# Performance work log

Measured on AMD Instinct MI355X. Metric: run time of the kernel, lower is better.

The kernel has to match this reference:

```python
import jax, jax.numpy as jnp
import numpy as np

N = 10000
E = 160000
IN_DIM = 128
HID = 128
HEADS = 8
INT_DIM = 512
OUT_DIM = 3
NEG_SLOPE = 0.2


def gat_conv(x, src, dst, W, a_src, a_dst, b, heads, ch):
    # x: [N, F_in]; W: [F_in, heads*ch]; a_src/a_dst: [heads, ch]; b: [heads*ch]
    n = x.shape[0]
    h = (x @ W).reshape(n, heads, ch)                      # [N,H,C]
    alpha_src = jnp.einsum('nhc,hc->nh', h, a_src)         # [N,H]
    alpha_dst = jnp.einsum('nhc,hc->nh', h, a_dst)         # [N,H]
    e = jax.nn.leaky_relu(alpha_src[src] + alpha_dst[dst], NEG_SLOPE)  # [E,H]
    # segment softmax over incoming edges of each dst node
    emax = jax.ops.segment_max(e, dst, num_segments=n)     # [N,H]
    ee = jnp.exp(e - emax[dst])
    denom = jax.ops.segment_sum(ee, dst, num_segments=n)   # [N,H]
    alpha = ee / (denom[dst] + 1e-16)                      # [E,H]
    msg = h[src] * alpha[:, :, None]                       # [E,H,C]
    out = jax.ops.segment_sum(msg, dst, num_segments=n)    # [N,H,C]
    return out.reshape(n, heads * ch) + b


def setup_inputs() -> dict:
    key = jax.random.key(0)
    ks = jax.random.split(key, 20)

    def glorot(k, shape):
        fan = shape[0] + shape[-1]
        s = jnp.sqrt(6.0 / fan)
        return jax.random.uniform(k, shape, jnp.float32, -s, s)

    x = jax.random.normal(ks[0], (N, IN_DIM), jnp.float32)
    edge_index = jax.random.randint(ks[1], (2, E), 0, N, jnp.int32)
    return {
        'x': x,
        'edge_index': edge_index,
        'W1': glorot(ks[2], (IN_DIM, HEADS * HID)),
        'a_src1': glorot(ks[3], (HEADS, HID)),
        'a_dst1': glorot(ks[4], (HEADS, HID)),
        'b1': jnp.zeros((HEADS * HID,), jnp.float32),
        'W2': glorot(ks[5], (HEADS * HID, HEADS * HID)),
        'a_src2': glorot(ks[6], (HEADS, HID)),
        'a_dst2': glorot(ks[7], (HEADS, HID)),
        'b2': jnp.zeros((HEADS * HID,), jnp.float32),
        'W3': glorot(ks[8], (HEADS * HID, INT_DIM)),
        'a_src3': glorot(ks[9], (1, INT_DIM)),
        'a_dst3': glorot(ks[10], (1, INT_DIM)),
        'b3': jnp.zeros((INT_DIM,), jnp.float32),
        'Wl': glorot(ks[11], (INT_DIM, INT_DIM)),
        'bl': jnp.zeros((INT_DIM,), jnp.float32),
        'Wc': glorot(ks[12], (INT_DIM, OUT_DIM)),
        'bc': jnp.zeros((OUT_DIM,), jnp.float32),
    }


def reference(x, edge_index, W1, a_src1, a_dst1, b1, W2, a_src2, a_dst2, b2,
              W3, a_src3, a_dst3, b3, Wl, bl, Wc, bc):
    src, dst = edge_index[0], edge_index[1]
    # eval mode: dropout_edge and Dropout are identity
    h = gat_conv(x, src, dst, W1, a_src1, a_dst1, b1, HEADS, HID)
    h = jax.nn.relu(h)
    h = gat_conv(h, src, dst, W2, a_src2, a_dst2, b2, HEADS, HID)
    h = jax.nn.relu(h)
    h = gat_conv(h, src, dst, W3, a_src3, a_dst3, b3, 1, INT_DIM)
    h = jax.nn.relu(h)
    h = jax.nn.relu(h @ Wl + bl)
    return h @ Wc + bc
```

## Files before the change

### kernel.cpp

```cpp
#include <hip/hip_runtime.h>
#include <hip/hip_bf16.h>

#define NN 10000
#define EE 160000
#define IN_DIM 128
#define HID 128
#define HEADS 8
#define F1 (HEADS*HID)
#define INT_DIM 512
#define OUT_DIM 3
#define MPAD 10112

typedef __attribute__((ext_vector_type(4))) float f32x4;
typedef __attribute__((ext_vector_type(8))) _Float16 half8;
typedef __attribute__((ext_vector_type(4))) _Float16 half4;
typedef __attribute__((ext_vector_type(2))) _Float16 half2v;

#define WAVE_SYNC() do { asm volatile("s_waitcnt lgkmcnt(0)" ::: "memory"); \
                         __builtin_amdgcn_sched_barrier(0); } while(0)

__global__ __launch_bounds__(256) void count_kernel(const int* __restrict__ dst, int E, int* __restrict__ cnt){
    int e = blockIdx.x*256 + threadIdx.x;
    if(e < E) atomicAdd(&cnt[dst[e]], 1);
}

__global__ __launch_bounds__(256) void scan_kernel(const int* __restrict__ cnt, int* __restrict__ rowp,
                                                   int* __restrict__ cursor, int n){
    __shared__ int sh[256];
    __shared__ int stotal;
    int t = threadIdx.x;
    if(t==0) stotal = 0;
    __syncthreads();
    for(int base=0; base<n; base+=256){
        int i = base + t;
        int v = (i<n) ? cnt[i] : 0;
        sh[t] = v;
        __syncthreads();
        #pragma unroll
        for(int off=1; off<256; off<<=1){
            int add = (t>=off) ? sh[t-off] : 0;
            __syncthreads();
            sh[t] += add;
            __syncthreads();
        }
        int excl = sh[t] - v;
        if(i<n){ rowp[i] = stotal + excl; cursor[i] = stotal + excl; }
        int chunk_total = sh[255];
        __syncthreads();
        if(t==0) stotal += chunk_total;
        __syncthreads();
    }
    if(t==0) rowp[n] = stotal;
}

__global__ __launch_bounds__(256) void fill_kernel(const int* __restrict__ src, const int* __restrict__ dst,
                                                   int E, int* __restrict__ cursor, int* __restrict__ colsrc){
    int e = blockIdx.x*256 + threadIdx.x;
    if(e < E){
        int d = dst[e];
        int pos = atomicAdd(&cursor[d], 1);
        colsrc[pos] = src[e];
    }
}

__global__ __launch_bounds__(256) void splitT16_kernel(const float* __restrict__ B, _Float16* __restrict__ T,
                                                       int K, int N){
    __shared__ float tile[32][33];
    const int tx = threadIdx.x & 31, ty = threadIdx.x >> 5;
    const int n0 = blockIdx.x * 32, k0 = blockIdx.y * 32;
    #pragma unroll
    for(int i = 0; i < 32; i += 8)
        tile[ty + i][tx] = B[(size_t)(k0 + ty + i) * N + n0 + tx];
    __syncthreads();
    #pragma unroll
    for(int i = 0; i < 32; i += 8){
        int n = ty + i;
        T[(size_t)(n0 + n) * K + k0 + tx] = (_Float16)tile[tx][n];
    }
}

__global__ __launch_bounds__(256) void x16_kernel(const float* __restrict__ x, _Float16* __restrict__ x16, int n4){
    int i = blockIdx.x*256 + threadIdx.x;
    if(i >= n4) return;
    float4 v = ((const float4*)x)[i];
    half4 o = { (_Float16)v.x, (_Float16)v.y, (_Float16)v.z, (_Float16)v.w };
    ((half4*)x16)[i] = o;
}

__global__ __launch_bounds__(256) void aw1_kernel(const float* __restrict__ W1,
                                                  const float* __restrict__ a_src,
                                                  const float* __restrict__ a_dst,
                                                  float* __restrict__ aw){
    int idx = blockIdx.x*256 + threadIdx.x;
    if(idx >= 16*IN_DIM) return;
    int j = idx >> 7, k = idx & 127;
    int hj = j & 7;
    const float* av = (j < 8 ? a_src : a_dst) + hj*HID;
    const float* wr = W1 + (size_t)k*F1 + hj*HID;
    float s = 0.f;
    #pragma unroll 4
    for(int c = 0; c < HID; c++) s += av[c] * wr[c];
    aw[idx] = s;
}

__global__ __launch_bounds__(256) void alpha1_kernel(const float* __restrict__ x,
                                                     const float* __restrict__ aw,
                                                     float* __restrict__ asrc, float* __restrict__ adst){
    __shared__ float xs[16][128];
    __shared__ float aws[16][128];
    int t = threadIdx.x;
    int nb = blockIdx.x * 16;
    for(int i = t; i < 16*128; i += 256){
        xs[i >> 7][i & 127] = x[(size_t)nb*128 + i];
        aws[i >> 7][i & 127] = aw[i];
    }
    __syncthreads();
    int nl = t >> 4, j = t & 15;
    float s = 0.f;
    #pragma unroll 4
    for(int c = 0; c < 128; c++) s += xs[nl][c] * aws[j][c];
    int node = nb + nl;
    if(j < 8) asrc[node*8 + j] = s;
    else      adst[node*8 + (j-8)] = s;
}

__global__ __launch_bounds__(256) void agg1_kernel(const _Float16* __restrict__ x16,
                                                   const float* __restrict__ asrc,
                                                   const float* __restrict__ adst,
                                                   const int* __restrict__ rowp,
                                                   const int* __restrict__ colsrc,
                                                   _Float16* __restrict__ oa){
    const int w = threadIdx.x >> 6, l = threadIdx.x & 63;
    const int node = blockIdx.x*4 + w;
    __shared__ float sh_ee[4][64][8];
    int beg = rowp[node], end = rowp[node+1];
    float rd = adst[node*8 + (l & 7)];
    float acc0[8], acc1[8];
    #pragma unroll
    for(int h=0;h<8;h++){ acc0[h]=0.f; acc1[h]=0.f; }
    float dpart = 0.f;
    for(int base=beg; base<end; base+=64){
        int clen = min(64, end-base);
        WAVE_SYNC();
        int sreg = (l < clen) ? colsrc[base + l] : 0;
        for(int it=l; it<clen*8; it+=64){
            int j = it >> 3;
            int s = colsrc[base + j];
            float e = asrc[s*8 + (l & 7)] + rd;
            e = (e > 0.f) ? e : 0.2f*e;
            float ee = expf(e);
            sh_ee[w][j][l & 7] = ee;
            dpart += ee;
        }
        WAVE_SYNC();
        #pragma unroll 2
        for(int j=0;j<clen;j++){
            int s = __shfl(sreg, j);
            half2v xv = ((const half2v*)(x16 + (size_t)s*128))[l];
            float x0 = (float)xv[0], x1 = (float)xv[1];
            #pragma unroll
            for(int h=0;h<8;h++){
                float wt = sh_ee[w][j][h];
                acc0[h] += wt * x0;
                acc1[h] += wt * x1;
            }
        }
    }
    dpart += __shfl_xor(dpart, 8);
    dpart += __shfl_xor(dpart, 16);
    dpart += __shfl_xor(dpart, 32);
    #pragma unroll
    for(int h=0;h<8;h++){
        float dn = __shfl(dpart, h) + 1e-16f;
        half2v o = { (_Float16)(acc0[h]/dn), (_Float16)(acc1[h]/dn) };
        *(half2v*)(oa + (size_t)node*F1 + h*128 + 2*l) = o;
    }
}

__global__ __launch_bounds__(256) void agg2_kernel(const _Float16* __restrict__ hbuf,
                                                   const float* __restrict__ asrc,
                                                   const float* __restrict__ adst,
                                                   const int* __restrict__ rowp,
                                                   const int* __restrict__ colsrc,
                                                   const float* __restrict__ bias,
                                                   _Float16* __restrict__ oa){
    const int w = threadIdx.x >> 6, l = threadIdx.x & 63;
    const int h = blockIdx.x & 7;
    const int node = (blockIdx.x >> 3)*4 + w;
    const int g = l >> 4, i = l & 15;
    int beg = rowp[node], end = rowp[node+1];
    float rd = adst[node*8 + h];
    float acc[8];
    #pragma unroll
    for(int k=0;k<8;k++) acc[k]=0.f;
    float dpart = 0.f;
    const _Float16* hb = hbuf + h*128 + 8*i;
    for(int base=beg; base<end; base+=64){
        int clen = min(64, end-base);
        int sreg = 0; float eereg = 0.f;
        if(l < clen){
            sreg = colsrc[base + l];
            float e = asrc[sreg*8 + h] + rd;
            e = (e > 0.f) ? e : 0.2f*e;
            eereg = expf(e);
            dpart += eereg;
        }
        int cpad = (clen + 3) & ~3;
        int s0 = __shfl(sreg, g);
        float w0 = __shfl(eereg, g);
        half8 v0 = *(const half8*)(hb + (size_t)s0*F1);
        #pragma unroll 1
        for(int j0=0; j0<cpad; j0+=4){
            half8 nv; float nw = 0.f;
            const bool more = (j0+4 < cpad);
            if(more){
                int ns = __shfl(sreg, j0+4+g);
                nw = __shfl(eereg, j0+4+g);
                nv = *(const half8*)(hb + (size_t)ns*F1);
            }
            #pragma unroll
            for(int k=0;k<8;k++) acc[k] += w0 * (float)v0[k];
            if(more){ v0 = nv; w0 = nw; }
        }
    }
    #pragma unroll
    for(int k=0;k<8;k++){
        acc[k] += __shfl_xor(acc[k], 16);
        acc[k] += __shfl_xor(acc[k], 32);
    }
    #pragma unroll
    for(int off=1; off<64; off<<=1) dpart += __shfl_xor(dpart, off);
    float dn = dpart + 1e-16f;
    if(g == 0){
        const int f = h*128 + 8*i;
        float4 b0 = *(const float4*)(bias + f);
        float4 b1 = *(const float4*)(bias + f + 4);
        float bb[8] = {b0.x,b0.y,b0.z,b0.w, b1.x,b1.y,b1.z,b1.w};
        half8 o;
        #pragma unroll
        for(int k=0;k<8;k++)
            o[k] = (_Float16)fmaxf(acc[k]/dn + bb[k], 0.f);
        *(half8*)(oa + (size_t)node*F1 + f) = o;
    }
}

__global__ __launch_bounds__(256) void agg3_kernel(const _Float16* __restrict__ hbuf,
                                                   const float* __restrict__ asrc,
                                                   const float* __restrict__ adst,
                                                   const int* __restrict__ rowp,
                                                   const int* __restrict__ colsrc,
                                                   const float* __restrict__ bias,
                                                   _Float16* __restrict__ oa){
    const int w = threadIdx.x >> 6, l = threadIdx.x & 63;
    const int i7 = blockIdx.x & 7;
    const int chunk = i7 & 3, sub = i7 >> 2;
    const int node = ((blockIdx.x >> 3)*2 + sub)*4 + w;
    const int g = l >> 4, i = l & 15;
    int beg = rowp[node], end = rowp[node+1];
    float rd = adst[node];
    float acc[8];
    #pragma unroll
    for(int k=0;k<8;k++) acc[k]=0.f;
    float dpart = 0.f;
    const _Float16* hb = hbuf + chunk*128 + 8*i;
    for(int base=beg; base<end; base+=64){
        int clen = min(64, end-base);
        int sreg = 0; float eereg = 0.f;
        if(l < clen){
            sreg = colsrc[base + l];
            float e = asrc[sreg] + rd;
            e = (e > 0.f) ? e : 0.2f*e;
            eereg = expf(e);
            dpart += eereg;
        }
        int cpad = (clen + 3) & ~3;
        int s0 = __shfl(sreg, g);
        float w0 = __shfl(eereg, g);
        half8 v0 = *(const half8*)(hb + (size_t)s0*INT_DIM);
        #pragma unroll 1
        for(int j0=0; j0<cpad; j0+=4){
            half8 nv; float nw = 0.f;
            const bool more = (j0+4 < cpad);
            if(more){
                int ns = __shfl(sreg, j0+4+g);
                nw = __shfl(eereg, j0+4+g);
                nv = *(const half8*)(hb + (size_t)ns*INT_DIM);
            }
            #pragma unroll
            for(int k=0;k<8;k++) acc[k] += w0 * (float)v0[k];
            if(more){ v0 = nv; w0 = nw; }
        }
    }
    #pragma unroll
    for(int k=0;k<8;k++){
        acc[k] += __shfl_xor(acc[k], 16);
        acc[k] += __shfl_xor(acc[k], 32);
    }
    #pragma unroll
    for(int off=1; off<64; off<<=1) dpart += __shfl_xor(dpart, off);
    float dn = dpart + 1e-16f;
    if(g == 0){
        const int f = chunk*128 + 8*i;
        float4 b0 = *(const float4*)(bias + f);
        float4 b1 = *(const float4*)(bias + f + 4);
        float bb[8] = {b0.x,b0.y,b0.z,b0.w, b1.x,b1.y,b1.z,b1.w};
        half8 o;
        #pragma unroll
        for(int k=0;k<8;k++)
            o[k] = (_Float16)fmaxf(acc[k]/dn + bb[k], 0.f);
        *(half8*)(oa + (size_t)node*INT_DIM + f) = o;
    }
}

template<int FUSE>
__global__ __launch_bounds__(512, 4) void mfma16_gemm_kernel(
    const _Float16* __restrict__ A, int lda, int za,
    const _Float16* __restrict__ B, int ldb, int zb,
    const float* __restrict__ bias, _Float16* __restrict__ O,
    int ldc, int zc, int K, int gx)
{
    __shared__ _Float16 lA[2][128*32];
    __shared__ _Float16 lB[2][128*32];
    const int tid  = threadIdx.x;
    const int lane = tid & 63;
    const int w    = tid >> 6;
    const int wm   = w >> 2;
    const int wn   = w & 3;
    const int z    = blockIdx.z;

    const int nwg = gridDim.x;
    const int q = nwg >> 3, r = nwg & 7;
    const int xcd = blockIdx.x & 7, idx = blockIdx.x >> 3;
    const int wgid = (xcd < r ? xcd*(q+1) : r*(q+1) + (xcd-r)*q) + idx;
    const int row0 = (wgid / gx) * 128, col0 = (wgid % gx) * 128;

    f32x4 acc[4][2];
    #pragma unroll
    for(int i=0;i<4;i++)
        #pragma unroll
        for(int j=0;j<2;j++) acc[i][j] = (f32x4){0.f,0.f,0.f,0.f};

    const int rr1 = tid >> 2;
    const int ss1 = (tid & 3) ^ ((rr1 >> 1) & 3);
    const size_t aoff = (size_t)(row0 + rr1) * lda + (size_t)z*za + ss1 * 8;
    const size_t boff = (size_t)(col0 + rr1) * ldb + (size_t)z*zb + ss1 * 8;

    typedef __attribute__((address_space(3))) char lds_char;
    lds_char* dA = (lds_char*)(&lA[0][0]) + w*1024;
    lds_char* dB = (lds_char*)(&lB[0][0]) + w*1024;

    int arow[4], brow[2];
    const int slotx = ((lane >> 4) ^ ((lane >> 1) & 3)) << 4;
    #pragma unroll
    for(int i=0;i<4;i++)
        arow[i] = (wm*64 + i*16 + (lane & 15)) * 64 + slotx;
    #pragma unroll
    for(int j=0;j<2;j++)
        brow[j] = (wn*32 + j*16 + (lane & 15)) * 64 + slotx;

    #define GLDS(src, dst) __builtin_amdgcn_global_load_lds( \
        (__attribute__((address_space(1))) void*)(src), \
        (__attribute__((address_space(3))) void*)(dst), 16, 0, 0)
    GLDS(A + aoff, dA);
    GLDS(B + boff, dB);
    __syncthreads();

    #pragma unroll 1
    for(int k0 = 0, kb = 0; k0 < K; k0 += 32, kb ^= 1){
        if(k0 + 32 < K){
            const int nb = kb ^ 1;
            GLDS(A + aoff + k0 + 32, dA + nb*8192);
            GLDS(B + boff + k0 + 32, dB + nb*8192);
        }
        const char* pA = (const char*)(&lA[0][0]) + kb*8192;
        const char* pB = (const char*)(&lB[0][0]) + kb*8192;
        half8 af[4];
        #pragma unroll
        for(int i=0;i<4;i++) af[i] = *(const half8*)(pA + arow[i]);
        #pragma unroll
        for(int j=0;j<2;j++){
            half8 bf = *(const half8*)(pB + brow[j]);
            #pragma unroll
            for(int i=0;i<4;i++)
                acc[i][j] = __builtin_amdgcn_mfma_f32_16x16x32_f16(af[i], bf, acc[i][j], 0, 0, 0);
        }
        __syncthreads();
    }
    #undef GLDS

    #pragma unroll
    for(int i=0;i<4;i++){
        const int rr = row0 + wm*64 + i*16 + ((lane >> 4) << 2);
        #pragma unroll
        for(int j=0;j<2;j++){
            const int gc = z*zc + col0 + wn*32 + j*16 + (lane & 15);
            float b = FUSE ? bias[gc] : 0.f;
            #pragma unroll
            for(int rg=0;rg<4;rg++){
                float v = acc[i][j][rg];
                if(FUSE) v = fmaxf(v + b, 0.f);
                O[(size_t)(rr + rg) * ldc + gc] = (_Float16)v;
            }
        }
    }
}

__global__ __launch_bounds__(128) void alpha16_h8_kernel(const _Float16* __restrict__ hbuf,
                                                         const float* __restrict__ a_src,
                                                         const float* __restrict__ a_dst,
                                                         float* __restrict__ asrc, float* __restrict__ adst){
    int node = blockIdx.x;
    int t = threadIdx.x;
    half8 v = ((const half8*)(hbuf + (size_t)node*F1))[t];
    const float4* ap = (const float4*)(a_src + 8*t);
    const float4* dp = (const float4*)(a_dst + 8*t);
    float4 a0 = ap[0], a1 = ap[1];
    float4 d0 = dp[0], d1 = dp[1];
    float av[8] = {a0.x,a0.y,a0.z,a0.w, a1.x,a1.y,a1.z,a1.w};
    float dv[8] = {d0.x,d0.y,d0.z,d0.w, d1.x,d1.y,d1.z,d1.w};
    float ps = 0.f, pd = 0.f;
    #pragma unroll
    for(int k=0;k<8;k++){
        float f = (float)v[k];
        ps += f * av[k];
        pd += f * dv[k];
    }
    #pragma unroll
    for(int off=8; off; off>>=1){ ps += __shfl_down(ps, off); pd += __shfl_down(pd, off); }
    if((t & 15) == 0){
        asrc[(size_t)node*8 + (t>>4)] = ps;
        adst[(size_t)node*8 + (t>>4)] = pd;
    }
}

__global__ __launch_bounds__(128) void alpha16_h1_kernel(const _Float16* __restrict__ hbuf,
                                                         const float* __restrict__ a_src,
                                                         const float* __restrict__ a_dst,
                                                         float* __restrict__ asrc, float* __restrict__ adst){
    int node = blockIdx.x;
    int t = threadIdx.x;
    half4 v = ((const half4*)(hbuf + (size_t)node*INT_DIM))[t];
    float4 a = ((const float4*)a_src)[t];
    float4 d = ((const float4*)a_dst)[t];
    float ps = (float)v[0]*a.x + (float)v[1]*a.y + (float)v[2]*a.z + (float)v[3]*a.w;
    float pd = (float)v[0]*d.x + (float)v[1]*d.y + (float)v[2]*d.z + (float)v[3]*d.w;
    #pragma unroll
    for(int off=32; off; off>>=1){ ps += __shfl_down(ps, off); pd += __shfl_down(pd, off); }
    __shared__ float shs[2], shd[2];
    int wv = t >> 6;
    if((t & 63) == 0){ shs[wv] = ps; shd[wv] = pd; }
    __syncthreads();
    if(t == 0){
        asrc[node] = shs[0] + shs[1];
        adst[node] = shd[0] + shd[1];
    }
}

__global__ __launch_bounds__(256) void cls16_kernel(const _Float16* __restrict__ h, const float* __restrict__ Wc,
                                                    const float* __restrict__ bc, float* __restrict__ out, int n){
    int node = blockIdx.x*4 + (threadIdx.x >> 6);
    int lane = threadIdx.x & 63;
    if(node >= n) return;
    half8 v = ((const half8*)(h + (size_t)node*INT_DIM))[lane];
    float s0=0.f, s1=0.f, s2=0.f;
    #pragma unroll
    for(int k=0;k<8;k++){
        float f = (float)v[k];
        const float* wr = Wc + (8*lane + k)*3;
        s0 += f * wr[0];
        s1 += f * wr[1];
        s2 += f * wr[2];
    }
    #pragma unroll
    for(int off=32; off; off>>=1){
        s0 += __shfl_down(s0, off);
        s1 += __shfl_down(s1, off);
        s2 += __shfl_down(s2, off);
    }
    if(lane==0){
        out[(size_t)node*3+0] = s0 + bc[0];
        out[(size_t)node*3+1] = s1 + bc[1];
        out[(size_t)node*3+2] = s2 + bc[2];
    }
}

extern "C" void kernel_launch(void* const* d_in, const int* in_sizes, int n_in,
                              void* d_out, int out_size, void* d_ws, size_t ws_size,
                              hipStream_t stream){
    const float* x      = (const float*)d_in[0];
    const int*   ei     = (const int*)d_in[1];
    const float* W1     = (const float*)d_in[2];
    const float* a_src1 = (const float*)d_in[3];
    const float* a_dst1 = (const float*)d_in[4];
    const float* b1     = (const float*)d_in[5];
    const float* W2     = (const float*)d_in[6];
    const float* a_src2 = (const float*)d_in[7];
    const float* a_dst2 = (const float*)d_in[8];
    const float* b2     = (const float*)d_in[9];
    const float* W3     = (const float*)d_in[10];
    const float* a_src3 = (const float*)d_in[11];
    const float* a_dst3 = (const float*)d_in[12];
    const float* b3     = (const float*)d_in[13];
    const float* Wl     = (const float*)d_in[14];
    const float* bl     = (const float*)d_in[15];
    const float* Wc     = (const float*)d_in[16];
    const float* bc     = (const float*)d_in[17];
    float* out = (float*)d_out;

    const int* src = ei;
    const int* dst = ei + EE;

    char* p = (char*)d_ws;
    char* regA = p;  p += (size_t)MPAD*F1*4;
    char* regB = p;  p += (size_t)MPAD*F1*4;
    _Float16* wt16 = (_Float16*)p;  p += (size_t)F1*F1*2;
    _Float16* x16  = (_Float16*)p;  p += (size_t)NN*IN_DIM*2;
    float* aw1  = (float*)p;  p += 16*IN_DIM*4;
    float* asrc = (float*)p;  p += (size_t)NN*HEADS*4;
    float* adst = (float*)p;  p += (size_t)NN*HEADS*4;
    int* cnt    = (int*)p;    p += NN*4;
    int* rowp   = (int*)p;    p += (NN+1)*4;
    int* cursor = (int*)p;    p += NN*4;
    int* colsrc = (int*)p;    p += EE*4;

    _Float16* hA = (_Float16*)regA;
    _Float16* hB = (_Float16*)regB;

    hipMemsetAsync(cnt, 0, NN*sizeof(int), stream);
    count_kernel<<<(EE+255)/256, 256, 0, stream>>>(dst, EE, cnt);
    scan_kernel<<<1, 256, 0, stream>>>(cnt, rowp, cursor, NN);
    fill_kernel<<<(EE+255)/256, 256, 0, stream>>>(src, dst, EE, cursor, colsrc);

    x16_kernel<<<(NN*IN_DIM/4 + 255)/256, 256, 0, stream>>>(x, x16, NN*IN_DIM/4);
    splitT16_kernel<<<dim3(F1/32, IN_DIM/32), 256, 0, stream>>>(W1, wt16, IN_DIM, F1);
    aw1_kernel<<<8, 256, 0, stream>>>(W1, a_src1, a_dst1, aw1);
    alpha1_kernel<<<NN/16, 256, 0, stream>>>(x, aw1, asrc, adst);
    agg1_kernel<<<NN/4, 256, 0, stream>>>(x16, asrc, adst, rowp, colsrc, hA);
    mfma16_gemm_kernel<1><<<dim3(MPAD/128, 1, HEADS), 512, 0, stream>>>(
        hA, F1, 128,  wt16, IN_DIM, 128*IN_DIM,
        b1, hB, F1, 128,  IN_DIM, 1);

    splitT16_kernel<<<dim3(F1/32, F1/32), 256, 0, stream>>>(W2, wt16, F1, F1);
    mfma16_gemm_kernel<0><<<dim3((F1/128)*(MPAD/128), 1, 1), 512, 0, stream>>>(
        hB, F1, 0,  wt16, F1, 0,
        nullptr, hA, F1, 0,  F1, F1/128);
    alpha16_h8_kernel<<<NN, 128, 0, stream>>>(hA, a_src2, a_dst2, asrc, adst);
    agg2_kernel<<<(NN/4)*8, 256, 0, stream>>>(hA, asrc, adst, rowp, colsrc, b2, hB);

    splitT16_kernel<<<dim3(INT_DIM/32, F1/32), 256, 0, stream>>>(W3, wt16, F1, INT_DIM);
    mfma16_gemm_kernel<0><<<dim3((INT_DIM/128)*(MPAD/128), 1, 1), 512, 0, stream>>>(
        hB, F1, 0,  wt16, F1, 0,
        nullptr, hA, INT_DIM, 0,  F1, INT_DIM/128);
    alpha16_h1_kernel<<<NN, 128, 0, stream>>>(hA, a_src3, a_dst3, asrc, adst);
    agg3_kernel<<<(NN/8)*8, 256, 0, stream>>>(hA, asrc, adst, rowp, colsrc, b3, hB);

    splitT16_kernel<<<dim3(INT_DIM/32, INT_DIM/32), 256, 0, stream>>>(Wl, wt16, INT_DIM, INT_DIM);
    mfma16_gemm_kernel<1><<<dim3((INT_DIM/128)*(MPAD/128), 1, 1), 512, 0, stream>>>(
        hB, INT_DIM, 0,  wt16, INT_DIM, 0,
        bl, hA, INT_DIM, 0,  INT_DIM, INT_DIM/128);

    cls16_kernel<<<(NN+3)/4, 256, 0, stream>>>(hA, Wc, bc, out, NN);
}
```

Measured before the change: 301.1 us.

## Fuse weight/input prep into one kernel and parallelize CSR scan

Merges the cnt memset, the x fp16 conversion, the attention-weight folding and all four weight transposes into one prep kernel launched up front. Each weight gets its own buffer placed in unused workspace. Replaces the serial chunked single-block scan with a 1024-thread scan that gives each thread ten elements and uses wave shuffles. This removes several launches and many block barriers, at the cost of holding more workspace for the pre-transposed weights.

```diff
diff --git a/kernel.cpp b/kernel.cpp
--- a/kernel.cpp
+++ b/kernel.cpp
@@ -24,33 +24,51 @@
     if(e < E) atomicAdd(&cnt[dst[e]], 1);
 }
 
-__global__ __launch_bounds__(256) void scan_kernel(const int* __restrict__ cnt, int* __restrict__ rowp,
-                                                   int* __restrict__ cursor, int n){
-    __shared__ int sh[256];
-    __shared__ int stotal;
+__global__ __launch_bounds__(1024) void scan_kernel(const int* __restrict__ cnt, int* __restrict__ rowp,
+                                                    int* __restrict__ cursor, int n){
     int t = threadIdx.x;
-    if(t==0) stotal = 0;
+    int base = t*10;
+    int vals[10];
+    int run = 0;
+    #pragma unroll
+    for(int k=0;k<10;k++){
+        int i = base+k;
+        int v = (i<n) ? cnt[i] : 0;
+        vals[k] = run;
+        run += v;
+    }
+    int lane = t & 63, wv = t >> 6;
+    int inc = run;
+    #pragma unroll
+    for(int off=1; off<64; off<<=1){
+        int u = __shfl_up(inc, off);
+        if(lane >= off) inc += u;
+    }
+    __shared__ int wtot[16], woff[16];
+    if(lane == 63) wtot[wv] = inc;
     __syncthreads();
-    for(int base=0; base<n; base+=256){
-        int i = base + t;
-        int v = (i<n) ? cnt[i] : 0;
-        sh[t] = v;
-        __syncthreads();
-        #pragma unroll
-        for(int off=1; off<256; off<<=1){
-            int add = (t>=off) ? sh[t-off] : 0;
-            __syncthreads();
-            sh[t] += add;
-            __syncthreads();
-        }
-        int excl = sh[t] - v;
-        if(i<n){ rowp[i] = stotal + excl; cursor[i] = stotal + excl; }
-        int chunk_total = sh[255];
-        __syncthreads();
-        if(t==0) stotal += chunk_total;
-        __syncthreads();
-    }
-    if(t==0) rowp[n] = stotal;
+    if(t < 16){
+        int v = wtot[t];
+        int inc2 = v;
+        #pragma unroll
+        for(int off=1; off<16; off<<=1){
+            int u = __shfl_up(inc2, off);
+            if(t >= off) inc2 += u;
+        }
+        woff[t] = inc2 - v;
+    }
+    __syncthreads();
+    int thread_excl = woff[wv] + inc - run;
+    #pragma unroll
+    for(int k=0;k<10;k++){
+        int i = base+k;
+        if(i<n){
+            int v = thread_excl + vals[k];
+            rowp[i] = v;
+            cursor[i] = v;
+        }
+    }
+    if(t == 1023) rowp[n] = thread_excl + run;
 }
 
 __global__ __launch_bounds__(256) void fill_kernel(const int* __restrict__ src, const int* __restrict__ dst,
@@ -63,44 +81,61 @@
     }
 }
 
-__global__ __launch_bounds__(256) void splitT16_kernel(const float* __restrict__ B, _Float16* __restrict__ T,
-                                                       int K, int N){
+__device__ inline void transpose_tile16(const float* __restrict__ B, _Float16* __restrict__ T,
+                                        int K, int N, int idx){
     __shared__ float tile[32][33];
     const int tx = threadIdx.x & 31, ty = threadIdx.x >> 5;
-    const int n0 = blockIdx.x * 32, k0 = blockIdx.y * 32;
+    const int gx = N >> 5;
+    const int n0 = (idx % gx) * 32, k0 = (idx / gx) * 32;
     #pragma unroll
     for(int i = 0; i < 32; i += 8)
         tile[ty + i][tx] = B[(size_t)(k0 + ty + i) * N + n0 + tx];
     __syncthreads();
     #pragma unroll
     for(int i = 0; i < 32; i += 8){
-        int n = ty + i;
-        T[(size_t)(n0 + n) * K + k0 + tx] = (_Float16)tile[tx][n];
-    }
-}
-
-__global__ __launch_bounds__(256) void x16_kernel(const float* __restrict__ x, _Float16* __restrict__ x16, int n4){
-    int i = blockIdx.x*256 + threadIdx.x;
-    if(i >= n4) return;
-    float4 v = ((const float4*)x)[i];
-    half4 o = { (_Float16)v.x, (_Float16)v.y, (_Float16)v.z, (_Float16)v.w };
-    ((half4*)x16)[i] = o;
-}
-
-__global__ __launch_bounds__(256) void aw1_kernel(const float* __restrict__ W1,
-                                                  const float* __restrict__ a_src,
-                                                  const float* __restrict__ a_dst,
-                                                  float* __restrict__ aw){
-    int idx = blockIdx.x*256 + threadIdx.x;
-    if(idx >= 16*IN_DIM) return;
-    int j = idx >> 7, k = idx & 127;
-    int hj = j & 7;
-    const float* av = (j < 8 ? a_src : a_dst) + hj*HID;
-    const float* wr = W1 + (size_t)k*F1 + hj*HID;
-    float s = 0.f;
-    #pragma unroll 4
-    for(int c = 0; c < HID; c++) s += av[c] * wr[c];
-    aw[idx] = s;
+        int nn = ty + i;
+        T[(size_t)(n0 + nn) * K + k0 + tx] = (_Float16)tile[tx][nn];
+    }
+}
+
+__global__ __launch_bounds__(256) void prep_kernel(
+    const float* __restrict__ W1, const float* __restrict__ W2,
+    const float* __restrict__ W3, const float* __restrict__ Wl,
+    const float* __restrict__ x,
+    const float* __restrict__ a_src1, const float* __restrict__ a_dst1,
+    _Float16* __restrict__ tW1, _Float16* __restrict__ tW2,
+    _Float16* __restrict__ tW3, _Float16* __restrict__ tWl,
+    _Float16* __restrict__ x16, float* __restrict__ aw,
+    int* __restrict__ cnt)
+{
+    int b = blockIdx.x;
+    if(b < 128){            transpose_tile16(W1, tW1, IN_DIM, F1, b); }
+    else if(b < 1152){      transpose_tile16(W2, tW2, F1, F1, b-128); }
+    else if(b < 1664){      transpose_tile16(W3, tW3, F1, INT_DIM, b-1152); }
+    else if(b < 1920){      transpose_tile16(Wl, tWl, INT_DIM, INT_DIM, b-1664); }
+    else if(b < 3170){
+        int i = (b-1920)*256 + threadIdx.x;
+        float4 v = ((const float4*)x)[i];
+        half4 o = { (_Float16)v.x, (_Float16)v.y, (_Float16)v.z, (_Float16)v.w };
+        ((half4*)x16)[i] = o;
+    }
+    else if(b < 3178){
+        int idx = (b-3170)*256 + threadIdx.x;
+        if(idx < 16*IN_DIM){
+            int j = idx >> 7, k = idx & 127;
+            int hj = j & 7;
+            const float* av = (j < 8 ? a_src1 : a_dst1) + hj*HID;
+            const float* wr = W1 + (size_t)k*F1 + hj*HID;
+            float s = 0.f;
+            #pragma unroll 4
+            for(int c = 0; c < HID; c++) s += av[c] * wr[c];
+            aw[idx] = s;
+        }
+    }
+    else {
+        int i = (b-3178)*1024 + threadIdx.x*4;
+        if(i < NN) *(int4*)(cnt + i) = (int4){0,0,0,0};
+    }
 }
 
 __global__ __launch_bounds__(256) void alpha1_kernel(const float* __restrict__ x,
@@ -513,8 +548,6 @@
     char* p = (char*)d_ws;
     char* regA = p;  p += (size_t)MPAD*F1*4;
     char* regB = p;  p += (size_t)MPAD*F1*4;
-    _Float16* wt16 = (_Float16*)p;  p += (size_t)F1*F1*2;
-    _Float16* x16  = (_Float16*)p;  p += (size_t)NN*IN_DIM*2;
     float* aw1  = (float*)p;  p += 16*IN_DIM*4;
     float* asrc = (float*)p;  p += (size_t)NN*HEADS*4;
     float* adst = (float*)p;  p += (size_t)NN*HEADS*4;
@@ -525,38 +558,39 @@
 
     _Float16* hA = (_Float16*)regA;
     _Float16* hB = (_Float16*)regB;
-
-    hipMemsetAsync(cnt, 0, NN*sizeof(int), stream);
+    _Float16* up   = (_Float16*)(regA + (size_t)MPAD*F1*2);
+    _Float16* tW1  = up;
+    _Float16* tW2  = tW1 + (size_t)F1*IN_DIM;
+    _Float16* tW3  = tW2 + (size_t)F1*F1;
+    _Float16* tWl  = tW3 + (size_t)INT_DIM*F1;
+    _Float16* x16  = tWl + (size_t)INT_DIM*INT_DIM;
+
+    prep_kernel<<<3188, 256, 0, stream>>>(W1, W2, W3, Wl, x, a_src1, a_dst1,
+                                          tW1, tW2, tW3, tWl, x16, aw1, cnt);
     count_kernel<<<(EE+255)/256, 256, 0, stream>>>(dst, EE, cnt);
-    scan_kernel<<<1, 256, 0, stream>>>(cnt, rowp, cursor, NN);
+    scan_kernel<<<1, 1024, 0, stream>>>(cnt, rowp, cursor, NN);
     fill_kernel<<<(EE+255)/256, 256, 0, stream>>>(src, dst, EE, cursor, colsrc);
 
-    x16_kernel<<<(NN*IN_DIM/4 + 255)/256, 256, 0, stream>>>(x, x16, NN*IN_DIM/4);
-    splitT16_kernel<<<dim3(F1/32, IN_DIM/32), 256, 0, stream>>>(W1, wt16, IN_DIM, F1);
-    aw1_kernel<<<8, 256, 0, stream>>>(W1, a_src1, a_dst1, aw1);
     alpha1_kernel<<<NN/16, 256, 0, stream>>>(x, aw1, asrc, adst);
     agg1_kernel<<<NN/4, 256, 0, stream>>>(x16, asrc, adst, rowp, colsrc, hA);
     mfma16_gemm_kernel<1><<<dim3(MPAD/128, 1, HEADS), 512, 0, stream>>>(
-        hA, F1, 128,  wt16, IN_DIM, 128*IN_DIM,
+        hA, F1, 128,  tW1, IN_DIM, 128*IN_DIM,
         b1, hB, F1, 128,  IN_DIM, 1);
 
-    splitT16_kernel<<<dim3(F1/32, F1/32), 256, 0, stream>>>(W2, wt16, F1, F1);
     mfma16_gemm_kernel<0><<<dim3((F1/128)*(MPAD/128), 1, 1), 512, 0, stream>>>(
-        hB, F1, 0,  wt16, F1, 0,
+        hB, F1, 0,  tW2, F1, 0,
         nullptr, hA, F1, 0,  F1, F1/128);
     alpha16_h8_kernel<<<NN, 128, 0, stream>>>(hA, a_src2, a_dst2, asrc, adst);
     agg2_kernel<<<(NN/4)*8, 256, 0, stream>>>(hA, asrc, adst, rowp, colsrc, b2, hB);
 
-    splitT16_kernel<<<dim3(INT_DIM/32, F1/32), 256, 0, stream>>>(W3, wt16, F1, INT_DIM);
     mfma16_gemm_kernel<0><<<dim3((INT_DIM/128)*(MPAD/128), 1, 1), 512, 0, stream>>>(
-        hB, F1, 0,  wt16, F1, 0,
+        hB, F1, 0,  tW3, F1, 0,
         nullptr, hA, INT_DIM, 0,  F1, INT_DIM/128);
     alpha16_h1_kernel<<<NN, 128, 0, stream>>>(hA, a_src3, a_dst3, asrc, adst);
     agg3_kernel<<<(NN/8)*8, 256, 0, stream>>>(hA, asrc, adst, rowp, colsrc, b3, hB);
 
-    splitT16_kernel<<<dim3(INT_DIM/32, INT_DIM/32), 256, 0, stream>>>(Wl, wt16, INT_DIM, INT_DIM);
     mfma16_gemm_kernel<1><<<dim3((INT_DIM/128)*(MPAD/128), 1, 1), 512, 0, stream>>>(
-        hB, INT_DIM, 0,  wt16, INT_DIM, 0,
+        hB, INT_DIM, 0,  tWl, INT_DIM, 0,
         bl, hA, INT_DIM, 0,  INT_DIM, INT_DIM/128);
 
     cls16_kernel<<<(NN+3)/4, 256, 0, stream>>>(hA, Wc, bc, out, NN);
```

Measured after the change: 251.6 us. 1.2x faster.
